# Optimization experiments

Measured on AMD Instinct MI355X. Metric: run time of the kernel, lower is better.

## Reference

```python
import jax, jax.numpy as jnp
import numpy as np
import math

SEQ, BSZ, D, H, W = 2048, 2, 1024, 16, 8
HD = D // H          # head_dim = 64
P = SEQ // W         # phrase_num = 256 (seq divisible by window -> no pad needed)


def setup_inputs() -> dict:
    key = jax.random.key(0)
    ks = jax.random.split(key, 8)
    s = 1.0 / math.sqrt(D)
    def w(k):
        return jax.random.normal(k, (D, D), jnp.float32) * s
    zb = jnp.zeros((D,), jnp.float32)
    return {
        'query': jax.random.normal(ks[0], (SEQ, BSZ, D), jnp.float32),
        'Wq_base': w(ks[1]), 'bq_base': zb,
        'Wk_base': w(ks[2]), 'bk_base': zb,
        'Wq_gauss': w(ks[3]), 'bq_gauss': zb,
        'Wk_gauss': w(ks[4]), 'bk_gauss': zb,
        'Wv': w(ks[5]), 'bv': zb,
        'Wo': w(ks[6]), 'bo': zb,
    }


def reference(query, Wq_base, bq_base, Wk_base, bk_base,
              Wq_gauss, bq_gauss, Wk_gauss, bk_gauss, Wv, bv, Wo, bo):
    seq, bsz, d = query.shape
    scaling = HD ** -0.5

    def to_heads(x):  # (len, bsz, D) -> (bsz, H, len, HD)
        return x.reshape(x.shape[0], bsz, H, HD).transpose(1, 2, 0, 3)

    # ---- base multi-head attention branch ----
    q_b = to_heads(query @ Wq_base.T + bq_base) * scaling
    k_b = to_heads(query @ Wk_base.T + bk_base)
    v = to_heads(query @ Wv.T + bv)
    base_scores = jnp.einsum('bhid,bhjd->bhij', q_b, k_b)   # (B,H,S,S)
    attn_base = jax.nn.softmax(base_scores, axis=-1)

    # ---- phrase encoding: fixed windows + max pooling ----
    phrase = query.reshape(P, W, bsz, d).max(axis=1)        # (P, bsz, D)

    # ---- gaussian branch: query attends over phrase reps ----
    q_g = to_heads(query @ Wq_gauss.T + bq_gauss) * scaling
    k_g = (phrase @ Wk_gauss.T + bk_gauss).reshape(P, bsz, H, HD).transpose(1, 2, 0, 3)
    wts = jax.nn.softmax(jnp.einsum('bhid,bhpd->bhip', q_g, k_g), axis=-1)  # (B,H,S,P)

    # fixed Gaussians per phrase: mu at window center, sigma = window/4
    pos = jnp.arange(seq, dtype=jnp.float32)                     # key positions
    mu = jnp.arange(P, dtype=jnp.float32) * W + (W - 1) / 2.0    # (P,)
    sigma = W / 4.0
    gauss = jnp.exp(-(pos[None, :] - mu[:, None]) ** 2 / (2.0 * sigma * sigma)) \
            / (math.sqrt(2.0 * math.pi) * sigma)                 # (P, S)
    attn_gauss = jnp.einsum('bhip,pj->bhij', wts, gauss)         # (B,H,S,S)

    # combine the two attention distributions
    attn = 0.5 * (attn_base + attn_gauss)

    out = jnp.einsum('bhij,bhjd->bhid', attn, v)                 # (B,H,S,HD)
    out = out.transpose(2, 0, 1, 3).reshape(seq, bsz, d)         # (S,B,D)
    return out @ Wo.T + bo
```

## Files before the change

kernel.cpp:

```cpp
#include <hip/hip_runtime.h>
#include <hip/hip_bf16.h>

#define SEQ 2048
#define BSZ 2
#define DIM 1024
#define NH 16
#define HD 64
#define WIN 8
#define PN 256

typedef __hip_bfloat16 bf16;
typedef __attribute__((ext_vector_type(8))) short short8;
typedef __attribute__((ext_vector_type(4))) float f32x4;

__device__ __forceinline__ float b2f(bf16 x) { return __bfloat162float(x); }
__device__ __forceinline__ bf16 f2b(float x) { return __float2bfloat16(x); }
__device__ __forceinline__ short fbits(float x) { bf16 h = __float2bfloat16(x); return *(short*)&h; }

__device__ __forceinline__ void gl_lds16(const bf16* g, bf16* l) {
    __builtin_amdgcn_global_load_lds((const __attribute__((address_space(1))) void*)g,
                                     (__attribute__((address_space(3))) void*)l, 16, 0, 0);
}

__global__ void convert_kernel(const float* __restrict__ q,
                               const float* __restrict__ w0, const float* __restrict__ w1,
                               const float* __restrict__ w2, const float* __restrict__ w3,
                               const float* __restrict__ w4, const float* __restrict__ w5,
                               const float* __restrict__ b0, const float* __restrict__ b1,
                               const float* __restrict__ b2, const float* __restrict__ b3,
                               const float* __restrict__ b4, const float* __restrict__ b5,
                               bf16* __restrict__ qbf, bf16* __restrict__ wbf,
                               float* __restrict__ bp) {
    int i = blockIdx.x * 256 + threadIdx.x;
    const int QV = (SEQ * BSZ * DIM) / 8;
    const int WV = (DIM * DIM) / 8;
    const int TV = QV + 6 * WV;
    if (i >= TV) {
        int j = i - TV;
        if (j >= 768) return;
        int mat = j >> 7, k = (j & 127) * 8;
        const float* s = (mat == 0) ? b0 : (mat == 1) ? b1 : (mat == 2) ? b2
                       : (mat == 3) ? b3 : (mat == 4) ? b4 : b5;
        *(f32x4*)(bp + mat * DIM + k)     = *(const f32x4*)(s + k);
        *(f32x4*)(bp + mat * DIM + k + 4) = *(const f32x4*)(s + k + 4);
        return;
    }
    const float* src;
    bf16* dst;
    size_t off;
    if (i < QV) { src = q; dst = qbf; off = (size_t)i * 8; }
    else {
        int j = i - QV;
        int mat = j / WV, k = j - mat * WV;
        src = (mat == 0) ? w0 : (mat == 1) ? w1 : (mat == 2) ? w2
            : (mat == 3) ? w3 : (mat == 4) ? w4 : w5;
        dst = wbf + (size_t)mat * DIM * DIM;
        off = (size_t)k * 8;
    }
    f32x4 av4 = *(const f32x4*)(src + off);
    f32x4 bv4 = *(const f32x4*)(src + off + 4);
    short8 o;
#pragma unroll
    for (int e = 0; e < 4; ++e) { o[e] = fbits(av4[e]); o[e + 4] = fbits(bv4[e]); }
    *(short8*)(dst + off) = o;
}

__global__ void phrase_max_kernel(const float* __restrict__ q, bf16* __restrict__ phrase) {
    int idx = blockIdx.x * 256 + threadIdx.x;
    int d  = idx % DIM;
    int pb = idx / DIM;
    int b  = pb % BSZ;
    int p  = pb / BSZ;
    float m = -1e30f;
#pragma unroll
    for (int w = 0; w < WIN; ++w)
        m = fmaxf(m, q[((size_t)(p * WIN + w) * BSZ + b) * DIM + d]);
    phrase[idx] = f2b(m);
}

__global__ void gauss_v_kernel(const bf16* __restrict__ vT, bf16* __restrict__ gvT) {
    int row = blockIdx.x;
    int p   = threadIdx.x;
    float mu = p * (float)WIN + (WIN - 1) * 0.5f;
    float acc = 0.f;
    int j0 = p * WIN - 12;
    const bf16* src = vT + (size_t)row * SEQ;
#pragma unroll
    for (int jj = 0; jj < 32; ++jj) {
        int j = j0 + jj;
        if (j < 0 || j >= SEQ) continue;
        float dd = (float)j - mu;
        acc += __expf(-dd * dd * 0.125f) * 0.199471140200716f * b2f(src[j]);
    }
    gvT[(size_t)row * PN + p] = f2b(acc);
}

__device__ __forceinline__ void gemm_body(const bf16* __restrict__ A,
                                          const bf16* __restrict__ W,
                                          const float* __restrict__ bias,
                                          void* __restrict__ Cout,
                                          int m0, int n0, float scale,
                                          int mode, int LEN) {
    __shared__ bf16 As[128 * 32];
    __shared__ bf16 Ws[128 * 32];
    int t = threadIdx.x;
    int wave = t >> 6, lane = t & 63;
    int wm = (wave >> 1) * 64, wn = (wave & 1) * 64;
    int l15 = lane & 15, quad = lane >> 4;

    f32x4 acc[4][4] = {};

    for (int k0 = 0; k0 < DIM; k0 += 32) {
        {
            int c0 = t, c1 = t + 256;
            gl_lds16(A + (size_t)(m0 + (c0 >> 2)) * DIM + k0 + (c0 & 3) * 8, &As[c0 * 8]);
            gl_lds16(A + (size_t)(m0 + (c1 >> 2)) * DIM + k0 + (c1 & 3) * 8, &As[c1 * 8]);
            gl_lds16(W + (size_t)(n0 + (c0 >> 2)) * DIM + k0 + (c0 & 3) * 8, &Ws[c0 * 8]);
            gl_lds16(W + (size_t)(n0 + (c1 >> 2)) * DIM + k0 + (c1 & 3) * 8, &Ws[c1 * 8]);
        }
        __syncthreads();
        short8 af[4], bfr[4];
#pragma unroll
        for (int tm = 0; tm < 4; ++tm)
            af[tm] = *(short8*)&As[(wm + tm * 16 + l15) * 32 + quad * 8];
#pragma unroll
        for (int tn = 0; tn < 4; ++tn)
            bfr[tn] = *(short8*)&Ws[(wn + tn * 16 + l15) * 32 + quad * 8];
#pragma unroll
        for (int tm = 0; tm < 4; ++tm)
#pragma unroll
            for (int tn = 0; tn < 4; ++tn)
                acc[tm][tn] = __builtin_amdgcn_mfma_f32_16x16x32_bf16(af[tm], bfr[tn], acc[tm][tn], 0, 0, 0);
        __syncthreads();
    }

#pragma unroll
    for (int tm = 0; tm < 4; ++tm) {
        int mrow = m0 + wm + tm * 16 + quad * 4;
#pragma unroll
        for (int tn = 0; tn < 4; ++tn) {
            int n = n0 + wn + tn * 16 + l15;
            float bsv = bias[n];
#pragma unroll
            for (int r = 0; r < 4; ++r) {
                int m = mrow + r;
                float val = (acc[tm][tn][r] + bsv) * scale;
                if (mode == 0) {
                    int s = m / BSZ, b = m % BSZ;
                    int h = n >> 6, hd = n & 63;
                    ((bf16*)Cout)[((size_t)(b * NH + h) * LEN + s) * HD + hd] = f2b(val);
                } else if (mode == 2) {
                    int s = m / BSZ, b = m % BSZ;
                    int h = n >> 6, hd = n & 63;
                    ((bf16*)Cout)[((size_t)(b * NH + h) * HD + hd) * LEN + s] = f2b(val);
                } else {
                    ((float*)Cout)[(size_t)m * DIM + n] = val;
                }
            }
        }
    }
}

#define QSCALE (0.125f * 1.44269504088896f)

__global__ __launch_bounds__(256) void gemm_proj(const bf16* __restrict__ qbf,
                                                 const bf16* __restrict__ phrasebf,
                                                 const bf16* __restrict__ wbf,
                                                 const float* __restrict__ bias_pack,
                                                 bf16* __restrict__ q_b, bf16* __restrict__ k_b,
                                                 bf16* __restrict__ vT, bf16* __restrict__ q_g,
                                                 bf16* __restrict__ k_g) {
    int z = blockIdx.z;
    const bf16* A = qbf;
    bf16* C;
    int mode = 0, LEN = SEQ;
    float scale = 1.0f;
    switch (z) {
        case 0: C = q_b; scale = QSCALE; break;
        case 1: C = k_b; break;
        case 2: C = vT; mode = 2; break;
        case 3: C = q_g; scale = QSCALE; break;
        default:
            if (blockIdx.x >= 4) return;
            A = phrasebf; C = k_g; LEN = PN; break;
    }
    gemm_body(A, wbf + (size_t)z * DIM * DIM, bias_pack + z * DIM, C,
              blockIdx.x * 128, blockIdx.y * 128, scale, mode, LEN);
}

__global__ __launch_bounds__(256) void gemm_final(const bf16* __restrict__ attn_bf,
                                                  const bf16* __restrict__ wbf,
                                                  const float* __restrict__ bias_pack,
                                                  float* __restrict__ out) {
    gemm_body(attn_bf, wbf + (size_t)5 * DIM * DIM, bias_pack + 5 * DIM, out,
              blockIdx.x * 128, blockIdx.y * 128, 1.0f, 1, SEQ);
}

__global__ __launch_bounds__(256) void attn_kernel(const bf16* __restrict__ qb,
                                                   const bf16* __restrict__ kb,
                                                   const bf16* __restrict__ vT,
                                                   const bf16* __restrict__ qg,
                                                   const bf16* __restrict__ kg,
                                                   const bf16* __restrict__ gvT,
                                                   bf16* __restrict__ out) {
    __shared__ bf16 Qs[128][72];
    __shared__ bf16 Ks[64][72];
    __shared__ bf16 Vt[64][72];
    __shared__ bf16 Ps[128][72];

    int t = threadIdx.x;
    int wave = t >> 6, lane = t & 63;
    int l15 = lane & 15, quad = lane >> 4;
    int q0 = blockIdx.x * 128;
    int bh = blockIdx.y;
    int b = bh / NH, h = bh % NH;

    const short8 ones = (short8)0x3F80;

    float result[2][4][4] = {};

    for (int phase = 0; phase < 2; ++phase) {
        const bf16* qptr = phase ? qb : qg;
        const bf16* kptr = phase ? kb : kg;
        const bf16* vtp  = phase ? vT : gvT;
        int kvlen = phase ? SEQ : PN;
        int nchunk = kvlen / 64;

        __syncthreads();
        {
            int r = t >> 1, c0 = (t & 1) * 32;
            const bf16* qsrc = qptr + ((size_t)bh * SEQ + q0 + r) * HD + c0;
#pragma unroll
            for (int e = 0; e < 4; ++e)
                *(short8*)&Qs[r][c0 + e * 8] = *(const short8*)(qsrc + e * 8);
        }

        int sr = t >> 2, sc = (t & 3) * 16;
        const bf16* kbase = kptr + ((size_t)bh * kvlen + sr) * HD + sc;
        const bf16* vbase = vtp + (size_t)(bh * HD + sr) * kvlen + sc;

        short8 kr0, kr1, vr0, vr1;
        kr0 = *(const short8*)(kbase);
        kr1 = *(const short8*)(kbase + 8);
        vr0 = *(const short8*)(vbase);
        vr1 = *(const short8*)(vbase + 8);

        f32x4 o_acc[2][4] = {};
        f32x4 l_acc[2] = {};
        for (int ch = 0; ch < nchunk; ++ch) {
            __syncthreads();
            *(short8*)&Ks[sr][sc]     = kr0;
            *(short8*)&Ks[sr][sc + 8] = kr1;
            *(short8*)&Vt[sr][sc]     = vr0;
            *(short8*)&Vt[sr][sc + 8] = vr1;
            if (ch + 1 < nchunk) {
                const bf16* kn = kbase + (size_t)(ch + 1) * 64 * HD;
                const bf16* vn = vbase + (ch + 1) * 64;
                kr0 = *(const short8*)(kn);
                kr1 = *(const short8*)(kn + 8);
                vr0 = *(const short8*)(vn);
                vr1 = *(const short8*)(vn + 8);
            }
            __syncthreads();

            f32x4 s_acc[2][4] = {};
#pragma unroll
            for (int kk = 0; kk < 2; ++kk) {
                short8 a0 = *(short8*)&Qs[wave * 32 + l15][kk * 32 + quad * 8];
                short8 a1 = *(short8*)&Qs[wave * 32 + 16 + l15][kk * 32 + quad * 8];
#pragma unroll
                for (int tn = 0; tn < 4; ++tn) {
                    short8 bb = *(short8*)&Ks[tn * 16 + l15][kk * 32 + quad * 8];
                    s_acc[0][tn] = __builtin_amdgcn_mfma_f32_16x16x32_bf16(a0, bb, s_acc[0][tn], 0, 0, 0);
                    s_acc[1][tn] = __builtin_amdgcn_mfma_f32_16x16x32_bf16(a1, bb, s_acc[1][tn], 0, 0, 0);
                }
            }
#pragma unroll
            for (int m = 0; m < 2; ++m)
#pragma unroll
                for (int tn = 0; tn < 4; ++tn)
#pragma unroll
                    for (int r = 0; r < 4; ++r)
                        Ps[wave * 32 + m * 16 + quad * 4 + r][tn * 16 + l15] =
                            f2b(exp2f(fminf(s_acc[m][tn][r], 43.f)));
#pragma unroll
            for (int kk = 0; kk < 2; ++kk) {
                short8 pa0 = *(short8*)&Ps[wave * 32 + l15][kk * 32 + quad * 8];
                short8 pa1 = *(short8*)&Ps[wave * 32 + 16 + l15][kk * 32 + quad * 8];
                l_acc[0] = __builtin_amdgcn_mfma_f32_16x16x32_bf16(pa0, ones, l_acc[0], 0, 0, 0);
                l_acc[1] = __builtin_amdgcn_mfma_f32_16x16x32_bf16(pa1, ones, l_acc[1], 0, 0, 0);
#pragma unroll
                for (int tn = 0; tn < 4; ++tn) {
                    short8 vb = *(short8*)&Vt[tn * 16 + l15][kk * 32 + quad * 8];
                    o_acc[0][tn] = __builtin_amdgcn_mfma_f32_16x16x32_bf16(pa0, vb, o_acc[0][tn], 0, 0, 0);
                    o_acc[1][tn] = __builtin_amdgcn_mfma_f32_16x16x32_bf16(pa1, vb, o_acc[1][tn], 0, 0, 0);
                }
            }
        }
#pragma unroll
        for (int m = 0; m < 2; ++m)
#pragma unroll
            for (int r = 0; r < 4; ++r) {
                float inv = 0.5f / fmaxf(l_acc[m][r], 1e-30f);
#pragma unroll
                for (int tn = 0; tn < 4; ++tn)
                    result[m][tn][r] += o_acc[m][tn][r] * inv;
            }
    }

#pragma unroll
    for (int m = 0; m < 2; ++m)
#pragma unroll
        for (int r = 0; r < 4; ++r) {
            int srow = q0 + wave * 32 + m * 16 + quad * 4 + r;
            int mm = srow * BSZ + b;
#pragma unroll
            for (int tn = 0; tn < 4; ++tn) {
                int dcol = h * HD + tn * 16 + l15;
                out[(size_t)mm * DIM + dcol] = f2b(result[m][tn][r]);
            }
        }
}

extern "C" void kernel_launch(void* const* d_in, const int* in_sizes, int n_in,
                              void* d_out, int out_size, void* d_ws, size_t ws_size,
                              hipStream_t stream) {
    (void)in_sizes; (void)n_in; (void)out_size; (void)ws_size;
    const float* query = (const float*)d_in[0];
    const float* Wq_b  = (const float*)d_in[1];
    const float* bq_b  = (const float*)d_in[2];
    const float* Wk_b  = (const float*)d_in[3];
    const float* bk_b  = (const float*)d_in[4];
    const float* Wq_g  = (const float*)d_in[5];
    const float* bq_g  = (const float*)d_in[6];
    const float* Wk_g  = (const float*)d_in[7];
    const float* bk_g  = (const float*)d_in[8];
    const float* Wv    = (const float*)d_in[9];
    const float* bv    = (const float*)d_in[10];
    const float* Wo    = (const float*)d_in[11];
    const float* bo    = (const float*)d_in[12];
    float* out = (float*)d_out;

    const size_t NQ = (size_t)BSZ * NH * SEQ * HD;
    const size_t NP = (size_t)BSZ * NH * PN * HD;
    bf16* qbf      = (bf16*)d_ws;
    bf16* wbf      = qbf + NQ;
    bf16* phrasebf = wbf + (size_t)6 * DIM * DIM;
    bf16* q_b      = phrasebf + (size_t)PN * BSZ * DIM;
    bf16* k_b      = q_b + NQ;
    bf16* vT       = k_b + NQ;
    bf16* q_g      = vT + NQ;
    bf16* k_g      = q_g + NQ;
    bf16* gvT      = k_g + NP;
    bf16* attn_bf  = gvT + NP;
    float* bias_pack = (float*)(attn_bf + NQ);

    const int QV = (SEQ * BSZ * DIM) / 8, WV6 = 6 * (DIM * DIM) / 8;
    convert_kernel<<<(QV + WV6) / 256 + 3, 256, 0, stream>>>(
        query, Wq_b, Wk_b, Wv, Wq_g, Wk_g, Wo,
        bq_b, bk_b, bv, bq_g, bk_g, bo, qbf, wbf, bias_pack);
    phrase_max_kernel<<<(PN * BSZ * DIM) / 256, 256, 0, stream>>>(query, phrasebf);

    dim3 gp((SEQ * BSZ) / 128, DIM / 128, 5);
    gemm_proj<<<gp, 256, 0, stream>>>(qbf, phrasebf, wbf, bias_pack,
                                      q_b, k_b, vT, q_g, k_g);

    gauss_v_kernel<<<BSZ * NH * HD, PN, 0, stream>>>(vT, gvT);

    dim3 g3(SEQ / 128, BSZ * NH);
    attn_kernel<<<g3, 256, 0, stream>>>(q_b, k_b, vT, q_g, k_g, gvT, attn_bf);

    dim3 gf((SEQ * BSZ) / 128, DIM / 128);
    gemm_final<<<gf, 256, 0, stream>>>(attn_bf, wbf, bias_pack, out);
}
```

Before: 325.0 us.

## Halve attention query tile, keep Q in registers, compute S transposed

The attention kernel now handles 64 query rows per block instead of 128, so each wave owns 16 rows and the grid has twice as many blocks. The Q fragments are loaded from LDS into registers once per phase instead of being reloaded every chunk. S is computed as K·Q^T so each lane holds four consecutive keys, which lets P be written to LDS as packed 4-element stores instead of scalar ones. The aim is more blocks and waves for latency hiding, fewer registers and less LDS traffic per wave. The cost is that K/V are staged and loaded twice as often per query row, and each wave issues fewer MFMAs per chunk.

```diff
diff --git a/kernel.cpp b/kernel.cpp
--- a/kernel.cpp
+++ b/kernel.cpp
@@ -11,6 +11,7 @@
 
 typedef __hip_bfloat16 bf16;
 typedef __attribute__((ext_vector_type(8))) short short8;
+typedef __attribute__((ext_vector_type(4))) short short4v;
 typedef __attribute__((ext_vector_type(4))) float f32x4;
 
 __device__ __forceinline__ float b2f(bf16 x) { return __bfloat162float(x); }
@@ -203,21 +204,21 @@
                                                    const bf16* __restrict__ kg,
                                                    const bf16* __restrict__ gvT,
                                                    bf16* __restrict__ out) {
-    __shared__ bf16 Qs[128][72];
+    __shared__ bf16 Qs[64][72];
     __shared__ bf16 Ks[64][72];
     __shared__ bf16 Vt[64][72];
-    __shared__ bf16 Ps[128][72];
+    __shared__ bf16 Ps[64][72];
 
     int t = threadIdx.x;
     int wave = t >> 6, lane = t & 63;
     int l15 = lane & 15, quad = lane >> 4;
-    int q0 = blockIdx.x * 128;
+    int q0 = blockIdx.x * 64;
     int bh = blockIdx.y;
     int b = bh / NH, h = bh % NH;
 
     const short8 ones = (short8)0x3F80;
 
-    float result[2][4][4] = {};
+    float result[4][4] = {};
 
     for (int phase = 0; phase < 2; ++phase) {
         const bf16* qptr = phase ? qb : qg;
@@ -228,25 +229,27 @@
 
         __syncthreads();
         {
-            int r = t >> 1, c0 = (t & 1) * 32;
+            int r = t >> 2, c0 = (t & 3) * 16;
             const bf16* qsrc = qptr + ((size_t)bh * SEQ + q0 + r) * HD + c0;
-#pragma unroll
-            for (int e = 0; e < 4; ++e)
-                *(short8*)&Qs[r][c0 + e * 8] = *(const short8*)(qsrc + e * 8);
-        }
+            *(short8*)&Qs[r][c0]     = *(const short8*)qsrc;
+            *(short8*)&Qs[r][c0 + 8] = *(const short8*)(qsrc + 8);
+        }
+        __syncthreads();
+        short8 bq[2];
+        bq[0] = *(short8*)&Qs[wave * 16 + l15][quad * 8];
+        bq[1] = *(short8*)&Qs[wave * 16 + l15][32 + quad * 8];
 
         int sr = t >> 2, sc = (t & 3) * 16;
         const bf16* kbase = kptr + ((size_t)bh * kvlen + sr) * HD + sc;
         const bf16* vbase = vtp + (size_t)(bh * HD + sr) * kvlen + sc;
 
-        short8 kr0, kr1, vr0, vr1;
-        kr0 = *(const short8*)(kbase);
-        kr1 = *(const short8*)(kbase + 8);
-        vr0 = *(const short8*)(vbase);
-        vr1 = *(const short8*)(vbase + 8);
-
-        f32x4 o_acc[2][4] = {};
-        f32x4 l_acc[2] = {};
+        short8 kr0 = *(const short8*)(kbase);
+        short8 kr1 = *(const short8*)(kbase + 8);
+        short8 vr0 = *(const short8*)(vbase);
+        short8 vr1 = *(const short8*)(vbase + 8);
+
+        f32x4 o_acc[4] = {};
+        f32x4 l_acc = {};
         for (int ch = 0; ch < nchunk; ++ch) {
             __syncthreads();
             *(short8*)&Ks[sr][sc]     = kr0;
@@ -263,63 +266,53 @@
             }
             __syncthreads();
 
-            f32x4 s_acc[2][4] = {};
+            f32x4 s_acc[4] = {};
 #pragma unroll
             for (int kk = 0; kk < 2; ++kk) {
-                short8 a0 = *(short8*)&Qs[wave * 32 + l15][kk * 32 + quad * 8];
-                short8 a1 = *(short8*)&Qs[wave * 32 + 16 + l15][kk * 32 + quad * 8];
 #pragma unroll
                 for (int tn = 0; tn < 4; ++tn) {
-                    short8 bb = *(short8*)&Ks[tn * 16 + l15][kk * 32 + quad * 8];
-                    s_acc[0][tn] = __builtin_amdgcn_mfma_f32_16x16x32_bf16(a0, bb, s_acc[0][tn], 0, 0, 0);
-                    s_acc[1][tn] = __builtin_amdgcn_mfma_f32_16x16x32_bf16(a1, bb, s_acc[1][tn], 0, 0, 0);
+                    short8 ak = *(short8*)&Ks[tn * 16 + l15][kk * 32 + quad * 8];
+                    s_acc[tn] = __builtin_amdgcn_mfma_f32_16x16x32_bf16(ak, bq[kk], s_acc[tn], 0, 0, 0);
                 }
             }
 #pragma unroll
-            for (int m = 0; m < 2; ++m)
-#pragma unroll
-                for (int tn = 0; tn < 4; ++tn)
-#pragma unroll
-                    for (int r = 0; r < 4; ++r)
-                        Ps[wave * 32 + m * 16 + quad * 4 + r][tn * 16 + l15] =
-                            f2b(exp2f(fminf(s_acc[m][tn][r], 43.f)));
+            for (int tn = 0; tn < 4; ++tn) {
+                short4v pk;
+#pragma unroll
+                for (int r = 0; r < 4; ++r)
+                    pk[r] = fbits(exp2f(fminf(s_acc[tn][r], 43.f)));
+                *(short4v*)&Ps[wave * 16 + l15][tn * 16 + quad * 4] = pk;
+            }
 #pragma unroll
             for (int kk = 0; kk < 2; ++kk) {
-                short8 pa0 = *(short8*)&Ps[wave * 32 + l15][kk * 32 + quad * 8];
-                short8 pa1 = *(short8*)&Ps[wave * 32 + 16 + l15][kk * 32 + quad * 8];
-                l_acc[0] = __builtin_amdgcn_mfma_f32_16x16x32_bf16(pa0, ones, l_acc[0], 0, 0, 0);
-                l_acc[1] = __builtin_amdgcn_mfma_f32_16x16x32_bf16(pa1, ones, l_acc[1], 0, 0, 0);
+                short8 pa = *(short8*)&Ps[wave * 16 + l15][kk * 32 + quad * 8];
+                l_acc = __builtin_amdgcn_mfma_f32_16x16x32_bf16(pa, ones, l_acc, 0, 0, 0);
 #pragma unroll
                 for (int tn = 0; tn < 4; ++tn) {
                     short8 vb = *(short8*)&Vt[tn * 16 + l15][kk * 32 + quad * 8];
-                    o_acc[0][tn] = __builtin_amdgcn_mfma_f32_16x16x32_bf16(pa0, vb, o_acc[0][tn], 0, 0, 0);
-                    o_acc[1][tn] = __builtin_amdgcn_mfma_f32_16x16x32_bf16(pa1, vb, o_acc[1][tn], 0, 0, 0);
+                    o_acc[tn] = __builtin_amdgcn_mfma_f32_16x16x32_bf16(pa, vb, o_acc[tn], 0, 0, 0);
                 }
             }
         }
 #pragma unroll
-        for (int m = 0; m < 2; ++m)
-#pragma unroll
-            for (int r = 0; r < 4; ++r) {
-                float inv = 0.5f / fmaxf(l_acc[m][r], 1e-30f);
-#pragma unroll
-                for (int tn = 0; tn < 4; ++tn)
-                    result[m][tn][r] += o_acc[m][tn][r] * inv;
-            }
-    }
-
-#pragma unroll
-    for (int m = 0; m < 2; ++m)
-#pragma unroll
         for (int r = 0; r < 4; ++r) {
-            int srow = q0 + wave * 32 + m * 16 + quad * 4 + r;
-            int mm = srow * BSZ + b;
-#pragma unroll
-            for (int tn = 0; tn < 4; ++tn) {
-                int dcol = h * HD + tn * 16 + l15;
-                out[(size_t)mm * DIM + dcol] = f2b(result[m][tn][r]);
-            }
-        }
+            float inv = 0.5f / fmaxf(l_acc[r], 1e-30f);
+#pragma unroll
+            for (int tn = 0; tn < 4; ++tn)
+                result[tn][r] += o_acc[tn][r] * inv;
+        }
+    }
+
+#pragma unroll
+    for (int r = 0; r < 4; ++r) {
+        int srow = q0 + wave * 16 + quad * 4 + r;
+        int mm = srow * BSZ + b;
+#pragma unroll
+        for (int tn = 0; tn < 4; ++tn) {
+            int dcol = h * HD + tn * 16 + l15;
+            out[(size_t)mm * DIM + dcol] = f2b(result[tn][r]);
+        }
+    }
 }
 
 extern "C" void kernel_launch(void* const* d_in, const int* in_sizes, int n_in,
@@ -367,7 +360,7 @@
 
     gauss_v_kernel<<<BSZ * NH * HD, PN, 0, stream>>>(vT, gvT);
 
-    dim3 g3(SEQ / 128, BSZ * NH);
+    dim3 g3(SEQ / 64, BSZ * NH);
     attn_kernel<<<g3, 256, 0, stream>>>(q_b, k_b, vT, q_g, k_g, gvT, attn_bf);
 
     dim3 gf((SEQ * BSZ) / 128, DIM / 128);
```

Measured after the change: 295.3 us. 1.1x faster.
